# Optimization experiments

Hardware: AMD Instinct MI355X
Metric: run time of the kernel (lower is better)

The kernel has to match this reference:

```python
import jax, jax.numpy as jnp
import numpy as np

B, L, H, E, V, Z, T = 256, 2, 1024, 256, 28, 1024, 512
SOS_IDX, EOS_IDX = 1, 0


def setup_inputs() -> dict:
    key = jax.random.key(0)
    ks = jax.random.split(key, 16)
    s = 0.05
    emb = s * jax.random.normal(ks[0], (V, E), jnp.float32)
    emb = emb.at[EOS_IDX].set(0.0)  # padding_idx=0
    return {
        "z": jax.random.normal(ks[1], (B, Z), jnp.float32),
        "emb": emb,
        "w_zh": s * jax.random.normal(ks[2], (L * H, Z), jnp.float32),
        "b_zh": jnp.zeros((L * H,), jnp.float32),
        "w_ih0": s * jax.random.normal(ks[3], (3 * H, E), jnp.float32),
        "w_hh0": s * jax.random.normal(ks[4], (3 * H, H), jnp.float32),
        "b_ih0": jnp.zeros((3 * H,), jnp.float32),
        "b_hh0": jnp.zeros((3 * H,), jnp.float32),
        "w_ih1": s * jax.random.normal(ks[5], (3 * H, H), jnp.float32),
        "w_hh1": s * jax.random.normal(ks[6], (3 * H, H), jnp.float32),
        "b_ih1": jnp.zeros((3 * H,), jnp.float32),
        "b_hh1": jnp.zeros((3 * H,), jnp.float32),
        "w_out": s * jax.random.normal(ks[7], (V, H), jnp.float32),
        "b_out": jnp.zeros((V,), jnp.float32),
    }


def _gru_cell(x, h, w_ih, w_hh, b_ih, b_hh):
    # PyTorch GRU cell math
    gi = x @ w_ih.T + b_ih          # [B, 3H]
    gh = h @ w_hh.T + b_hh          # [B, 3H]
    i_r, i_z, i_n = jnp.split(gi, 3, axis=-1)
    h_r, h_z, h_n = jnp.split(gh, 3, axis=-1)
    r = jax.nn.sigmoid(i_r + h_r)
    zg = jax.nn.sigmoid(i_z + h_z)
    n = jnp.tanh(i_n + r * h_n)
    return (1.0 - zg) * n + zg * h


def reference(z, emb, w_zh, b_zh, w_ih0, w_hh0, b_ih0, b_hh0,
              w_ih1, w_hh1, b_ih1, b_hh1, w_out, b_out):
    # init hidden from latent: (B, L*H) -> per-layer (B, H)
    h = jnp.tanh(z @ w_zh.T + b_zh).reshape(-1, L, H)
    h0, h1 = h[:, 0, :], h[:, 1, :]
    tok0 = jnp.full((z.shape[0],), SOS_IDX, jnp.int32)
    keys = jax.random.split(jax.random.key(42), T)

    def step(carry, k):
        tok, h0, h1 = carry
        x = emb[tok]                         # [B, E] embedding lookup
        h0n = _gru_cell(x, h0, w_ih0, w_hh0, b_ih0, b_hh0)
        h1n = _gru_cell(h0n, h1, w_ih1, w_hh1, b_ih1, b_hh1)
        logit = h1n @ w_out.T + b_out        # [B, V]
        tok_n = jax.random.categorical(k, logit)  # multinomial(softmax(logit))
        return (tok_n, h0n, h1n), (logit, tok_n)

    _, (logits, tokens) = jax.lax.scan(step, (tok0, h0, h1), keys)
    # [T, B, V] -> [B, T, V]; [T, B] -> [B, T]
    return logits.transpose(1, 0, 2), tokens.T
```

## Files before the change

kernel.cpp:

```cpp
#include <hip/hip_runtime.h>

#define BB 256
#define HH 1024
#define EE 256
#define VV 28
#define ZZ 1024
#define TT 512
#define G3 3072
#define NTHR 256
#define TOKBASE (BB * TT * VV)

#define BM 64
#define BN 64
#define KT 32

typedef float f4 __attribute__((ext_vector_type(4)));
typedef float f32x4 __attribute__((ext_vector_type(4)));
typedef _Float16 f16x8 __attribute__((ext_vector_type(8)));
typedef unsigned short u16x4 __attribute__((ext_vector_type(4)));
typedef unsigned short u16x8 __attribute__((ext_vector_type(8)));

#define RES_SCALE 512.0f
#define INV_RES (1.0f / 512.0f)

__device__ __align__(16) float g_h0[2][BB][HH];
__device__ __align__(16) float g_h1[2][BB][HH];
__device__ __align__(16) float g_gh0b[BB][G3];
__device__ __align__(16) float g_gh1b[BB][G3];
__device__ __align__(16) float g_gi1[BB][G3];
__device__ __align__(16) float g_P0[VV][G3];
__device__ __align__(16) unsigned short g_h0t[32][2][4][BB][8];
__device__ __align__(16) unsigned short g_h1t[32][2][4][BB][8];
__device__ __align__(16) unsigned short g_wt[3][48][32][2][4][64][8];

__device__ __forceinline__ uint2 tf2x32(unsigned k0, unsigned k1,
                                        unsigned x0, unsigned x1) {
  unsigned ks2 = k0 ^ k1 ^ 0x1BD11BDAu;
  unsigned ksl[3] = {k0, k1, ks2};
  x0 += k0; x1 += k1;
#pragma unroll
  for (int g = 0; g < 5; ++g) {
    const int r0 = (g & 1) ? 17 : 13;
    const int r1 = (g & 1) ? 29 : 15;
    const int r2 = (g & 1) ? 16 : 26;
    const int r3 = (g & 1) ? 24 : 6;
    x0 += x1; x1 = (x1 << r0) | (x1 >> (32 - r0)); x1 ^= x0;
    x0 += x1; x1 = (x1 << r1) | (x1 >> (32 - r1)); x1 ^= x0;
    x0 += x1; x1 = (x1 << r2) | (x1 >> (32 - r2)); x1 ^= x0;
    x0 += x1; x1 = (x1 << r3) | (x1 >> (32 - r3)); x1 ^= x0;
    x0 += ksl[(g + 1) % 3];
    x1 += ksl[(g + 2) % 3] + (unsigned)(g + 1);
  }
  return make_uint2(x0, x1);
}

__device__ __forceinline__ float sigf(float x) {
  return 1.0f / (1.0f + expf(-x));
}

__device__ __forceinline__ float gru_h(float i_r, float h_r, float i_z, float h_z,
                                       float i_n, float h_n, float hprev) {
  float r  = sigf(i_r + h_r);
  float zg = sigf(i_z + h_z);
  float n  = tanhf(i_n + r * h_n);
  return (1.0f - zg) * n + zg * hprev;
}

__device__ __forceinline__ void split2(float x, unsigned short& a,
                                       unsigned short& b) {
  _Float16 h1 = (_Float16)x;
  _Float16 h2 = (_Float16)((x - (float)h1) * RES_SCALE);
  a = __builtin_bit_cast(unsigned short, h1);
  b = __builtin_bit_cast(unsigned short, h2);
}

__device__ __forceinline__ void gload16(unsigned short* l, const unsigned short* g) {
  __builtin_amdgcn_global_load_lds(
      (const __attribute__((address_space(1))) unsigned int*)(g),
      (__attribute__((address_space(3))) unsigned int*)(l), 16, 0, 0);
}

__device__ __forceinline__ void gemm_unit(
    const float* __restrict__ At, int lda, int rows_valid,
    const float* __restrict__ Wt, int ldw,
    const float* __restrict__ bias,
    float* __restrict__ Ct, int ldc,
    int K, int mode,
    float (&As)[BM][KT + 4], float (&Ws)[KT][BN + 4]) {
  const int tid = threadIdx.x;
  const int tx = tid & 15, ty = tid >> 4;
  f4 acc0 = {0.f, 0.f, 0.f, 0.f};
  f4 acc1 = {0.f, 0.f, 0.f, 0.f};
  f4 acc2 = {0.f, 0.f, 0.f, 0.f};
  f4 acc3 = {0.f, 0.f, 0.f, 0.f};

  for (int kb = 0; kb < K; kb += KT) {
#pragma unroll
    for (int l = 0; l < 2; ++l) {
      int f = tid + l * NTHR;
      int r = f >> 3, kq = (f & 7) << 2;
      f4 v = {0.f, 0.f, 0.f, 0.f};
      if (r < rows_valid) v = *(const f4*)(At + r * lda + kb + kq);
      *(f4*)&As[r][kq] = v;
    }
#pragma unroll
    for (int l = 0; l < 2; ++l) {
      int f = tid + l * NTHR;
      int nr = f >> 3, kq = (f & 7) << 2;
      f4 v = *(const f4*)(Wt + nr * ldw + kb + kq);
      Ws[kq + 0][nr] = v[0];
      Ws[kq + 1][nr] = v[1];
      Ws[kq + 2][nr] = v[2];
      Ws[kq + 3][nr] = v[3];
    }
    __syncthreads();
#pragma unroll
    for (int kk = 0; kk < KT; kk += 4) {
      f4 a0 = *(const f4*)&As[(ty << 2) + 0][kk];
      f4 a1 = *(const f4*)&As[(ty << 2) + 1][kk];
      f4 a2 = *(const f4*)&As[(ty << 2) + 2][kk];
      f4 a3 = *(const f4*)&As[(ty << 2) + 3][kk];
      f4 b0 = *(const f4*)&Ws[kk + 0][tx << 2];
      f4 b1 = *(const f4*)&Ws[kk + 1][tx << 2];
      f4 b2 = *(const f4*)&Ws[kk + 2][tx << 2];
      f4 b3 = *(const f4*)&Ws[kk + 3][tx << 2];
      acc0 += b0 * a0[0]; acc0 += b1 * a0[1]; acc0 += b2 * a0[2]; acc0 += b3 * a0[3];
      acc1 += b0 * a1[0]; acc1 += b1 * a1[1]; acc1 += b2 * a1[2]; acc1 += b3 * a1[3];
      acc2 += b0 * a2[0]; acc2 += b1 * a2[1]; acc2 += b2 * a2[2]; acc2 += b3 * a2[3];
      acc3 += b0 * a3[0]; acc3 += b1 * a3[1]; acc3 += b2 * a3[2]; acc3 += b3 * a3[3];
    }
    __syncthreads();
  }

  f4 accs[4] = {acc0, acc1, acc2, acc3};
#pragma unroll
  for (int i = 0; i < 4; ++i) {
    int r = (ty << 2) + i;
    if (r < rows_valid) {
#pragma unroll
      for (int j = 0; j < 4; ++j) {
        int c = (tx << 2) + j;
        float v = accs[i][j] + bias[c];
        if (mode == 1) v = tanhf(v);
        Ct[r * ldc + c] = v;
      }
    }
  }
}

#define A_CH (2 * 4 * 128)
#define W_CH (2 * 4 * 64)
#define BUFSZ ((A_CH + W_CH) * 8)

__device__ __forceinline__ void mm_tile(
    const unsigned short* __restrict__ At,
    const unsigned short* __restrict__ Wt,
    const float* __restrict__ bias,
    float* __restrict__ C,
    int m0, int n0, unsigned short* lds) {
  const int tid = threadIdx.x;
  const int w = tid >> 6, lane = tid & 63;
  const int wr = w >> 1, wc = w & 1;
  const int lr = lane & 15, lk8 = lane >> 4;

  f32x4 acc1[4][2] = {};
  f32x4 accR[4][2] = {};

  auto stage = [&](int buf, int ks) {
    unsigned short* lA = lds + buf * BUFSZ;
    unsigned short* lW = lA + A_CH * 8;
    const unsigned short* abase = At + (size_t)ks * (2 * 4 * BB * 8);
#pragma unroll
    for (int r = 0; r < 4; ++r) {
      int j = r * NTHR + tid;
      int skk = j >> 7, row = j & 127;
      gload16(lA + j * 8, abase + ((size_t)skk * BB + m0 + row) * 8);
    }
    const unsigned short* wbase = Wt + (size_t)ks * (2 * 4 * 64 * 8);
#pragma unroll
    for (int r = 0; r < 2; ++r) {
      int j = r * NTHR + tid;
      gload16(lW + j * 8, wbase + j * 8);
    }
  };

  stage(0, 0);
  int cur = 0;
  for (int ks = 0; ks < HH / 32; ++ks) {
    __syncthreads();
    if (ks + 1 < HH / 32) stage(cur ^ 1, ks + 1);
    const unsigned short* lA = lds + cur * BUFSZ;
    const unsigned short* lW = lA + A_CH * 8;
    f16x8 a[4][2], b[2][2];
#pragma unroll
    for (int mi = 0; mi < 4; ++mi)
#pragma unroll
      for (int s = 0; s < 2; ++s)
        a[mi][s] = *(const f16x8*)(lA + (((s << 2) | lk8) * 128 + wr * 64 + mi * 16 + lr) * 8);
#pragma unroll
    for (int ni = 0; ni < 2; ++ni)
#pragma unroll
      for (int s = 0; s < 2; ++s)
        b[ni][s] = *(const f16x8*)(lW + (((s << 2) | lk8) * 64 + wc * 32 + ni * 16 + lr) * 8);
#pragma unroll
    for (int mi = 0; mi < 4; ++mi)
#pragma unroll
      for (int ni = 0; ni < 2; ++ni) {
        acc1[mi][ni] = __builtin_amdgcn_mfma_f32_16x16x32_f16(a[mi][0], b[ni][0], acc1[mi][ni], 0, 0, 0);
        accR[mi][ni] = __builtin_amdgcn_mfma_f32_16x16x32_f16(a[mi][0], b[ni][1], accR[mi][ni], 0, 0, 0);
        accR[mi][ni] = __builtin_amdgcn_mfma_f32_16x16x32_f16(a[mi][1], b[ni][0], accR[mi][ni], 0, 0, 0);
      }
    cur ^= 1;
  }

#pragma unroll
  for (int mi = 0; mi < 4; ++mi) {
    int rowb = m0 + wr * 64 + mi * 16 + ((lane >> 4) << 2);
#pragma unroll
    for (int ni = 0; ni < 2; ++ni) {
      int col = n0 + wc * 32 + ni * 16 + lr;
      float bv = bias[col];
#pragma unroll
      for (int r = 0; r < 4; ++r)
        C[(size_t)(rowb + r) * G3 + col] = acc1[mi][ni][r] + accR[mi][ni][r] * INV_RES + bv;
    }
  }
}

__device__ __forceinline__ void write_ht(unsigned short (*ht)[2][4][BB][8],
                                         int row, int k0,
                                         u16x4 o1, u16x4 o2) {
  const int ks = k0 >> 5, kk = (k0 >> 3) & 3, e0 = k0 & 7;
  *(u16x4*)&ht[ks][0][kk][row][e0] = o1;
  *(u16x4*)&ht[ks][1][kk][row][e0] = o2;
}

__global__ __launch_bounds__(NTHR) void k_setup1(
    const float* __restrict__ z, const float* __restrict__ w_zh,
    const float* __restrict__ b_zh, const float* __restrict__ emb,
    const float* __restrict__ w_ih0, const float* __restrict__ b_ih0) {
  __shared__ __align__(16) float As[BM][KT + 4];
  __shared__ __align__(16) float Ws[KT][BN + 4];
  const int bid = blockIdx.x;
  if (bid < 128) {
    int m0 = (bid >> 5) * BM;
    int n0 = (bid & 31) * BN;
    float* Cb;
    int col;
    if (n0 < HH) { Cb = &g_h0[1][0][0]; col = n0; }
    else         { Cb = &g_h1[1][0][0]; col = n0 - HH; }
    gemm_unit(z + m0 * ZZ, ZZ, BM, w_zh + n0 * ZZ, ZZ, b_zh + n0,
              Cb + m0 * HH + col, HH, ZZ, 1, As, Ws);
  } else {
    int n0 = (bid - 128) * BN;
    gemm_unit(emb, EE, VV, w_ih0 + n0 * EE, EE, b_ih0 + n0,
              &g_P0[0][0] + n0, G3, EE, 0, As, Ws);
  }
}

__global__ __launch_bounds__(NTHR) void k_splitw(
    const float* __restrict__ w_ih1, const float* __restrict__ w_hh0,
    const float* __restrict__ w_hh1) {
  unsigned u = blockIdx.x * NTHR + threadIdx.x;
  int row = u & 63, kk = (u >> 6) & 3, ks = (u >> 8) & 31, rem = u >> 13;
  int mat = rem / 48, bn = rem % 48;
  const float* src = (mat == 0) ? w_ih1 : (mat == 1) ? w_hh0 : w_hh1;
  const float* p = src + (size_t)(bn * 64 + row) * HH + ks * 32 + kk * 8;
  f4 v0 = *(const f4*)p;
  f4 v1 = *(const f4*)(p + 4);
  u16x8 o1, o2;
#pragma unroll
  for (int c = 0; c < 8; ++c) {
    float x = (c < 4) ? v0[c] : v1[c - 4];
    unsigned short a, b;
    split2(x, a, b);
    o1[c] = a; o2[c] = b;
  }
  *(u16x8*)&g_wt[mat][bn][ks][0][kk][row][0] = o1;
  *(u16x8*)&g_wt[mat][bn][ks][1][kk][row][0] = o2;
}

__global__ __launch_bounds__(NTHR) void k_splith() {
  unsigned e = blockIdx.x * NTHR + threadIdx.x;
  int mat = e >> 16, r = (e >> 8) & 255, k0 = (e & 255) << 2;
  const float* src = (mat == 0) ? &g_h0[1][0][0] : &g_h1[1][0][0];
  f4 v = *(const f4*)(src + (size_t)r * HH + k0);
  u16x4 o1, o2;
#pragma unroll
  for (int c = 0; c < 4; ++c) {
    unsigned short a, b;
    split2(v[c], a, b);
    o1[c] = a; o2[c] = b;
  }
  write_ht((mat == 0) ? g_h0t : g_h1t, r, k0, o1, o2);
}

__global__ __launch_bounds__(NTHR, 2) void k_mm_init(const float* __restrict__ b_hh0) {
  __shared__ __align__(16) unsigned short lds[2 * BUFSZ];
  int bm = blockIdx.x / 48, bn = blockIdx.x % 48;
  mm_tile(&g_h0t[0][0][0][0][0], &g_wt[1][bn][0][0][0][0][0], b_hh0,
          &g_gh0b[0][0], bm * 128, bn * 64, lds);
}

__global__ __launch_bounds__(NTHR) void k_gate0_init() {
  const int b = blockIdx.x, tid = threadIdx.x, j = tid << 2;
  const float* __restrict__ gi = g_P0[1];
  const float* __restrict__ gh = g_gh0b[b];
  f4 ir = *(const f4*)&gi[j];
  f4 iz = *(const f4*)&gi[j + HH];
  f4 in_ = *(const f4*)&gi[j + 2 * HH];
  f4 hr = *(const f4*)&gh[j];
  f4 hz = *(const f4*)&gh[j + HH];
  f4 hn = *(const f4*)&gh[j + 2 * HH];
  f4 hp = *(const f4*)&g_h0[1][b][j];
  f4 ho;
  u16x4 o1, o2;
#pragma unroll
  for (int c = 0; c < 4; ++c) {
    ho[c] = gru_h(ir[c], hr[c], iz[c], hz[c], in_[c], hn[c], hp[c]);
    unsigned short a, bb2;
    split2(ho[c], a, bb2);
    o1[c] = a; o2[c] = bb2;
  }
  *(f4*)&g_h0[0][b][j] = ho;
  write_ht(g_h0t, b, j, o1, o2);
}

__global__ __launch_bounds__(NTHR, 2) void k_mm(
    const float* __restrict__ b_ih1, const float* __restrict__ b_hh0,
    const float* __restrict__ b_hh1) {
  __shared__ __align__(16) unsigned short lds[2 * BUFSZ];
  const int bid = blockIdx.x;
  const int mat = bid / 96, v = bid % 96;
  const int m0 = (v / 48) * 128, bn = v % 48, n0 = bn * 64;
  const unsigned short* At = (mat == 2) ? &g_h1t[0][0][0][0][0] : &g_h0t[0][0][0][0][0];
  const unsigned short* Wt = &g_wt[mat][bn][0][0][0][0][0];
  const float* bias = (mat == 0) ? b_ih1 : (mat == 1) ? b_hh0 : b_hh1;
  float* C = (mat == 0) ? &g_gi1[0][0] : (mat == 1) ? &g_gh0b[0][0] : &g_gh1b[0][0];
  mm_tile(At, Wt, bias, C, m0, n0, lds);
}

__global__ __launch_bounds__(NTHR) void k_fuse(
    int t, const float* __restrict__ w_out, const float* __restrict__ b_out,
    float* __restrict__ out) {
  __shared__ __align__(16) float s_h[HH];
  __shared__ float s_log[32];
  __shared__ float s_score[32];
  __shared__ int s_tok;
  const int b = blockIdx.x, tid = threadIdx.x, j = tid << 2;
  const int pw = t & 1, pr = pw ^ 1;

  {
    const float* __restrict__ gi = g_gi1[b];
    const float* __restrict__ gh = g_gh1b[b];
    f4 ir = *(const f4*)&gi[j];
    f4 iz = *(const f4*)&gi[j + HH];
    f4 in_ = *(const f4*)&gi[j + 2 * HH];
    f4 hr = *(const f4*)&gh[j];
    f4 hz = *(const f4*)&gh[j + HH];
    f4 hn = *(const f4*)&gh[j + 2 * HH];
    f4 hp = *(const f4*)&g_h1[pr][b][j];
    f4 ho;
    u16x4 o1, o2;
#pragma unroll
    for (int c = 0; c < 4; ++c) {
      ho[c] = gru_h(ir[c], hr[c], iz[c], hz[c], in_[c], hn[c], hp[c]);
      unsigned short a, bb2;
      split2(ho[c], a, bb2);
      o1[c] = a; o2[c] = bb2;
    }
    *(f4*)&g_h1[pw][b][j] = ho;
    *(f4*)&s_h[j] = ho;
    write_ht(g_h1t, b, j, o1, o2);
  }
  __syncthreads();

  {
    const int v = tid >> 3, ks = tid & 7;
    float part = 0.f;
    if (v < VV) {
      const float* __restrict__ wrow = w_out + v * HH + ks * 128;
      const float* __restrict__ hh = s_h + ks * 128;
#pragma unroll 8
      for (int i = 0; i < 128; i += 4) {
        f4 wv = *(const f4*)&wrow[i];
        f4 hv = *(const f4*)&hh[i];
        part += hv[0] * wv[0] + hv[1] * wv[1] + hv[2] * wv[2] + hv[3] * wv[3];
      }
    }
    part += __shfl_xor(part, 1);
    part += __shfl_xor(part, 2);
    part += __shfl_xor(part, 4);
    if (v < VV && ks == 0) s_log[v] = part;
  }
  __syncthreads();

  if (tid < VV) {
    float logit = s_log[tid] + b_out[tid];
    out[(size_t)b * (TT * VV) + (size_t)t * VV + tid] = logit;
    uint2 kt = tf2x32(0u, 42u, 0u, (unsigned)t);
    uint2 rr = tf2x32(kt.x, kt.y, 0u, (unsigned)(b * VV + tid));
    unsigned bits = rr.x ^ rr.y;
    float uf = __uint_as_float((bits >> 9) | 0x3f800000u) - 1.0f;
    if (uf <= 0.0f) uf = 1.17549435e-38f;
    s_score[tid] = logit - logf(-logf(uf));
  }
  __syncthreads();
  if (tid == 0) {
    float best = s_score[0];
    int bv = 0;
    for (int vv = 1; vv < VV; ++vv) {
      float s = s_score[vv];
      if (s > best) { best = s; bv = vv; }
    }
    s_tok = bv;
    out[TOKBASE + (size_t)b * TT + t] = (float)bv;
  }
  __syncthreads();

  {
    const int tok = s_tok;
    const float* __restrict__ gi = g_P0[tok];
    const float* __restrict__ gh = g_gh0b[b];
    f4 ir = *(const f4*)&gi[j];
    f4 iz = *(const f4*)&gi[j + HH];
    f4 in_ = *(const f4*)&gi[j + 2 * HH];
    f4 hr = *(const f4*)&gh[j];
    f4 hz = *(const f4*)&gh[j + HH];
    f4 hn = *(const f4*)&gh[j + 2 * HH];
    f4 hp = *(const f4*)&g_h0[pw][b][j];
    f4 ho;
    u16x4 o1, o2;
#pragma unroll
    for (int c = 0; c < 4; ++c) {
      ho[c] = gru_h(ir[c], hr[c], iz[c], hz[c], in_[c], hn[c], hp[c]);
      unsigned short a, bb2;
      split2(ho[c], a, bb2);
      o1[c] = a; o2[c] = bb2;
    }
    *(f4*)&g_h0[pr][b][j] = ho;
    write_ht(g_h0t, b, j, o1, o2);
  }
}

extern "C" void kernel_launch(void* const* d_in, const int* in_sizes, int n_in,
                              void* d_out, int out_size, void* d_ws, size_t ws_size,
                              hipStream_t stream) {
  (void)in_sizes; (void)n_in; (void)d_ws; (void)ws_size; (void)out_size;
  const float* z     = (const float*)d_in[0];
  const float* emb   = (const float*)d_in[1];
  const float* w_zh  = (const float*)d_in[2];
  const float* b_zh  = (const float*)d_in[3];
  const float* w_ih0 = (const float*)d_in[4];
  const float* w_hh0 = (const float*)d_in[5];
  const float* b_ih0 = (const float*)d_in[6];
  const float* b_hh0 = (const float*)d_in[7];
  const float* w_ih1 = (const float*)d_in[8];
  const float* w_hh1 = (const float*)d_in[9];
  const float* b_ih1 = (const float*)d_in[10];
  const float* b_hh1 = (const float*)d_in[11];
  const float* w_out = (const float*)d_in[12];
  const float* b_out = (const float*)d_in[13];
  float* out = (float*)d_out;

  k_setup1<<<dim3(176), dim3(NTHR), 0, stream>>>(z, w_zh, b_zh, emb, w_ih0, b_ih0);
  k_splitw<<<dim3(4608), dim3(NTHR), 0, stream>>>(w_ih1, w_hh0, w_hh1);
  k_splith<<<dim3(512), dim3(NTHR), 0, stream>>>();
  k_mm_init<<<dim3(96), dim3(NTHR), 0, stream>>>(b_hh0);
  k_gate0_init<<<dim3(BB), dim3(NTHR), 0, stream>>>();

  for (int t = 0; t < TT; ++t) {
    k_mm<<<dim3(288), dim3(NTHR), 0, stream>>>(b_ih1, b_hh0, b_hh1);
    k_fuse<<<dim3(BB), dim3(NTHR), 0, stream>>>(t, w_out, b_out, out);
  }
}
```

Measured before the change: 16.96 ms.

## Retile recurrent GEMM to full-batch 256x48 tiles, 192 blocks

Changes the per-step MFMA GEMM tiling from 128x64 tiles (288 blocks) to tiles covering the full batch of 256 rows by 48 columns (192 blocks). Each wave now owns 64 rows and all 48 columns, and the weight split layout is regenerated to match. The aim is to load each weight tile once per step instead of twice across the batch, and to reduce the block count to fit the 256 CUs in a single wave. The cost is a larger LDS buffer, more accumulators per thread, and fewer blocks, which may lower occupancy and latency hiding.

```diff
diff --git a/kernel.cpp b/kernel.cpp
--- a/kernel.cpp
+++ b/kernel.cpp
@@ -14,6 +14,9 @@
 #define BN 64
 #define KT 32
 
+#define MMN 48
+#define NBN 64
+
 typedef float f4 __attribute__((ext_vector_type(4)));
 typedef float f32x4 __attribute__((ext_vector_type(4)));
 typedef _Float16 f16x8 __attribute__((ext_vector_type(8)));
@@ -31,7 +34,7 @@
 __device__ __align__(16) float g_P0[VV][G3];
 __device__ __align__(16) unsigned short g_h0t[32][2][4][BB][8];
 __device__ __align__(16) unsigned short g_h1t[32][2][4][BB][8];
-__device__ __align__(16) unsigned short g_wt[3][48][32][2][4][64][8];
+__device__ __align__(16) unsigned short g_wt[3][NBN][32][2][4][MMN][8];
 
 __device__ __forceinline__ uint2 tf2x32(unsigned k0, unsigned k1,
                                         unsigned x0, unsigned x1) {
@@ -148,8 +151,8 @@
   }
 }
 
-#define A_CH (2 * 4 * 128)
-#define W_CH (2 * 4 * 64)
+#define A_CH (2 * 4 * 256)
+#define W_CH (2 * 4 * MMN)
 #define BUFSZ ((A_CH + W_CH) * 8)
 
 __device__ __forceinline__ void mm_tile(
@@ -157,30 +160,28 @@
     const unsigned short* __restrict__ Wt,
     const float* __restrict__ bias,
     float* __restrict__ C,
-    int m0, int n0, unsigned short* lds) {
+    int n0, unsigned short* lds) {
   const int tid = threadIdx.x;
-  const int w = tid >> 6, lane = tid & 63;
-  const int wr = w >> 1, wc = w & 1;
+  const int wr = tid >> 6, lane = tid & 63;
   const int lr = lane & 15, lk8 = lane >> 4;
 
-  f32x4 acc1[4][2] = {};
-  f32x4 accR[4][2] = {};
+  f32x4 acc1[4][3] = {};
+  f32x4 accR[4][3] = {};
 
   auto stage = [&](int buf, int ks) {
     unsigned short* lA = lds + buf * BUFSZ;
     unsigned short* lW = lA + A_CH * 8;
-    const unsigned short* abase = At + (size_t)ks * (2 * 4 * BB * 8);
-#pragma unroll
-    for (int r = 0; r < 4; ++r) {
+    const unsigned short* abase = At + (size_t)ks * (A_CH * 8);
+#pragma unroll
+    for (int r = 0; r < 8; ++r) {
       int j = r * NTHR + tid;
-      int skk = j >> 7, row = j & 127;
-      gload16(lA + j * 8, abase + ((size_t)skk * BB + m0 + row) * 8);
-    }
-    const unsigned short* wbase = Wt + (size_t)ks * (2 * 4 * 64 * 8);
-#pragma unroll
-    for (int r = 0; r < 2; ++r) {
-      int j = r * NTHR + tid;
-      gload16(lW + j * 8, wbase + j * 8);
+      gload16(lA + j * 8, abase + (size_t)j * 8);
+    }
+    const unsigned short* wbase = Wt + (size_t)ks * (W_CH * 8);
+    gload16(lW + tid * 8, wbase + (size_t)tid * 8);
+    if (tid < W_CH - NTHR) {
+      int j = NTHR + tid;
+      gload16(lW + j * 8, wbase + (size_t)j * 8);
     }
   };
 
@@ -191,21 +192,21 @@
     if (ks + 1 < HH / 32) stage(cur ^ 1, ks + 1);
     const unsigned short* lA = lds + cur * BUFSZ;
     const unsigned short* lW = lA + A_CH * 8;
-    f16x8 a[4][2], b[2][2];
+    f16x8 a[4][2], b[3][2];
 #pragma unroll
     for (int mi = 0; mi < 4; ++mi)
 #pragma unroll
       for (int s = 0; s < 2; ++s)
-        a[mi][s] = *(const f16x8*)(lA + (((s << 2) | lk8) * 128 + wr * 64 + mi * 16 + lr) * 8);
-#pragma unroll
-    for (int ni = 0; ni < 2; ++ni)
+        a[mi][s] = *(const f16x8*)(lA + (((s << 2) | lk8) * 256 + wr * 64 + mi * 16 + lr) * 8);
+#pragma unroll
+    for (int ni = 0; ni < 3; ++ni)
 #pragma unroll
       for (int s = 0; s < 2; ++s)
-        b[ni][s] = *(const f16x8*)(lW + (((s << 2) | lk8) * 64 + wc * 32 + ni * 16 + lr) * 8);
+        b[ni][s] = *(const f16x8*)(lW + (((s << 2) | lk8) * MMN + ni * 16 + lr) * 8);
 #pragma unroll
     for (int mi = 0; mi < 4; ++mi)
 #pragma unroll
-      for (int ni = 0; ni < 2; ++ni) {
+      for (int ni = 0; ni < 3; ++ni) {
         acc1[mi][ni] = __builtin_amdgcn_mfma_f32_16x16x32_f16(a[mi][0], b[ni][0], acc1[mi][ni], 0, 0, 0);
         accR[mi][ni] = __builtin_amdgcn_mfma_f32_16x16x32_f16(a[mi][0], b[ni][1], accR[mi][ni], 0, 0, 0);
         accR[mi][ni] = __builtin_amdgcn_mfma_f32_16x16x32_f16(a[mi][1], b[ni][0], accR[mi][ni], 0, 0, 0);
@@ -215,10 +216,10 @@
 
 #pragma unroll
   for (int mi = 0; mi < 4; ++mi) {
-    int rowb = m0 + wr * 64 + mi * 16 + ((lane >> 4) << 2);
-#pragma unroll
-    for (int ni = 0; ni < 2; ++ni) {
-      int col = n0 + wc * 32 + ni * 16 + lr;
+    int rowb = wr * 64 + mi * 16 + ((lane >> 4) << 2);
+#pragma unroll
+    for (int ni = 0; ni < 3; ++ni) {
+      int col = n0 + ni * 16 + lr;
       float bv = bias[col];
 #pragma unroll
       for (int r = 0; r < 4; ++r)
@@ -262,10 +263,13 @@
     const float* __restrict__ w_ih1, const float* __restrict__ w_hh0,
     const float* __restrict__ w_hh1) {
   unsigned u = blockIdx.x * NTHR + threadIdx.x;
-  int row = u & 63, kk = (u >> 6) & 3, ks = (u >> 8) & 31, rem = u >> 13;
-  int mat = rem / 48, bn = rem % 48;
+  int row = u % MMN;
+  unsigned v = u / MMN;
+  int kk = v & 3, ks = (v >> 2) & 31;
+  unsigned rem = v >> 7;
+  int mat = rem / NBN, bn = rem % NBN;
   const float* src = (mat == 0) ? w_ih1 : (mat == 1) ? w_hh0 : w_hh1;
-  const float* p = src + (size_t)(bn * 64 + row) * HH + ks * 32 + kk * 8;
+  const float* p = src + (size_t)(bn * MMN + row) * HH + ks * 32 + kk * 8;
   f4 v0 = *(const f4*)p;
   f4 v1 = *(const f4*)(p + 4);
   u16x8 o1, o2;
@@ -297,9 +301,9 @@
 
 __global__ __launch_bounds__(NTHR, 2) void k_mm_init(const float* __restrict__ b_hh0) {
   __shared__ __align__(16) unsigned short lds[2 * BUFSZ];
-  int bm = blockIdx.x / 48, bn = blockIdx.x % 48;
+  int bn = blockIdx.x;
   mm_tile(&g_h0t[0][0][0][0][0], &g_wt[1][bn][0][0][0][0][0], b_hh0,
-          &g_gh0b[0][0], bm * 128, bn * 64, lds);
+          &g_gh0b[0][0], bn * MMN, lds);
 }
 
 __global__ __launch_bounds__(NTHR) void k_gate0_init() {
@@ -331,13 +335,12 @@
     const float* __restrict__ b_hh1) {
   __shared__ __align__(16) unsigned short lds[2 * BUFSZ];
   const int bid = blockIdx.x;
-  const int mat = bid / 96, v = bid % 96;
-  const int m0 = (v / 48) * 128, bn = v % 48, n0 = bn * 64;
+  const int mat = bid >> 6, bn = bid & 63;
   const unsigned short* At = (mat == 2) ? &g_h1t[0][0][0][0][0] : &g_h0t[0][0][0][0][0];
   const unsigned short* Wt = &g_wt[mat][bn][0][0][0][0][0];
   const float* bias = (mat == 0) ? b_ih1 : (mat == 1) ? b_hh0 : b_hh1;
   float* C = (mat == 0) ? &g_gi1[0][0] : (mat == 1) ? &g_gh0b[0][0] : &g_gh1b[0][0];
-  mm_tile(At, Wt, bias, C, m0, n0, lds);
+  mm_tile(At, Wt, bias, C, bn * MMN, lds);
 }
 
 __global__ __launch_bounds__(NTHR) void k_fuse(
@@ -466,11 +469,11 @@
   k_setup1<<<dim3(176), dim3(NTHR), 0, stream>>>(z, w_zh, b_zh, emb, w_ih0, b_ih0);
   k_splitw<<<dim3(4608), dim3(NTHR), 0, stream>>>(w_ih1, w_hh0, w_hh1);
   k_splith<<<dim3(512), dim3(NTHR), 0, stream>>>();
-  k_mm_init<<<dim3(96), dim3(NTHR), 0, stream>>>(b_hh0);
+  k_mm_init<<<dim3(64), dim3(NTHR), 0, stream>>>(b_hh0);
   k_gate0_init<<<dim3(BB), dim3(NTHR), 0, stream>>>();
 
   for (int t = 0; t < TT; ++t) {
-    k_mm<<<dim3(288), dim3(NTHR), 0, stream>>>(b_ih1, b_hh0, b_hh1);
+    k_mm<<<dim3(192), dim3(NTHR), 0, stream>>>(b_ih1, b_hh0, b_hh1);
     k_fuse<<<dim3(BB), dim3(NTHR), 0, stream>>>(t, w_out, b_out, out);
   }
 }
```

After: 18.14 ms. +7.0%, slower.
